# Performance work log

Measured on AMD Instinct MI355X. Metric: run time of the kernel, lower is better.

## Reference

```python
import jax, jax.numpy as jnp
import numpy as np

B, S = 2, 2048
D, H, L = 768, 12, 2
DH = D // H
WIN = 128            # one-sided sliding window
C = WIN              # query chunk size
NC = S // C
FF = 4 * D
V = 50265
SEP_ID = 2
NSEP = 16
G = NSEP + 1         # CLS + all SEP tokens are global
NCLS = 7
HID = 100
NEG = -1e9
SEP_POS = np.arange(1, NSEP + 1) * 120   # fixed [SEP] layout, same every row


def setup_inputs() -> dict:
    key = jax.random.key(0)
    ks = iter(jax.random.split(key, 32))
    def p(shape, scale=0.02):
        return scale * jax.random.normal(next(ks), shape, jnp.float32)
    input_ids = jax.random.randint(next(ks), (B, S), 10, V)
    input_ids = input_ids.at[:, SEP_POS].set(SEP_ID)
    attention_mask = jnp.ones((B, S), jnp.int32)
    return dict(
        input_ids=input_ids, attention_mask=attention_mask,
        tok_emb=p((V, D)), pos_emb=p((S, D)),
        ln_e_g=jnp.ones((D,)), ln_e_b=jnp.zeros((D,)),
        Wq=p((L, D, D)), bq=jnp.zeros((L, D)),
        Wk=p((L, D, D)), bk=jnp.zeros((L, D)),
        Wv=p((L, D, D)), bv=jnp.zeros((L, D)),
        Wo=p((L, D, D)), bo=jnp.zeros((L, D)),
        ln1_g=jnp.ones((L, D)), ln1_b=jnp.zeros((L, D)),
        W1=p((L, D, FF)), b1=jnp.zeros((L, FF)),
        W2=p((L, FF, D)), b2=jnp.zeros((L, D)),
        ln2_g=jnp.ones((L, D)), ln2_b=jnp.zeros((L, D)),
        Wh=p((2 * D, HID)), bh=jnp.zeros((HID,)),
        Wout=p((HID, NCLS)), bout=jnp.zeros((NCLS,)),
    )


def _ln(x, g, b):
    mu = jnp.mean(x, -1, keepdims=True)
    var = jnp.var(x, -1, keepdims=True)
    return (x - mu) * jax.lax.rsqrt(var + 1e-5) * g + b


def forward(input_ids, attention_mask, tok_emb, pos_emb, ln_e_g, ln_e_b,
            Wq, bq, Wk, bk, Wv, bv, Wo, bo, ln1_g, ln1_b,
            W1, b1, W2, b2, ln2_g, ln2_b, Wh, bh, Wout, bout):
    # global positions: CLS + every [SEP] (same layout in every row)
    sep_pos = jnp.nonzero(input_ids[0] == SEP_ID, size=NSEP)[0]          # [NSEP]
    glob = jnp.concatenate([jnp.zeros((1,), sep_pos.dtype), sep_pos])    # [G]

    amask = attention_mask.astype(jnp.float32)                           # [B,S]
    is_glob = jnp.zeros((S,), bool).at[glob].set(True)

    # banded (sliding-window) gather pattern, padded-coordinate indices
    idx = jnp.arange(NC)[:, None] * C + jnp.arange(3 * C)[None, :]       # [NC,3C]
    pos_k = idx - C                                                      # abs key pos
    pos_q = jnp.arange(NC)[:, None] * C + jnp.arange(C)[None, :]         # [NC,C]
    pos_k_c = jnp.clip(pos_k, 0, S - 1)
    band = jnp.abs(pos_k[:, None, :] - pos_q[:, :, None]) <= WIN         # [NC,C,3C]
    inb = (pos_k >= 0) & (pos_k < S)                                     # [NC,3C]
    # global keys are handled by the dedicated global columns -> drop from band
    band = band & (inb & ~is_glob[pos_k_c])[:, None, :]
    km = amask[:, pos_k_c] * inb                                         # [B,NC,3C]
    valid = band[None] & (km[:, :, None, :] > 0)                         # [B,NC,C,3C]
    gmask = amask[:, glob] > 0                                           # [B,G]

    x = tok_emb[input_ids] + pos_emb[None]                               # [B,S,D]
    x = _ln(x, ln_e_g, ln_e_b)

    for l in range(L):
        q = (x @ Wq[l] + bq[l]).reshape(B, S, H, DH).transpose(0, 2, 1, 3) * (DH ** -0.5)
        k = (x @ Wk[l] + bk[l]).reshape(B, S, H, DH).transpose(0, 2, 1, 3)
        v = (x @ Wv[l] + bv[l]).reshape(B, S, H, DH).transpose(0, 2, 1, 3)
        kp = jnp.pad(k, ((0, 0), (0, 0), (C, C), (0, 0)))
        vp = jnp.pad(v, ((0, 0), (0, 0), (C, C), (0, 0)))
        k3 = kp[:, :, idx]                                               # [B,H,NC,3C,DH]
        v3 = vp[:, :, idx]
        qc = q.reshape(B, H, NC, C, DH)
        s_loc = jnp.einsum('bhncd,bhnkd->bhnck', qc, k3)                 # banded scores
        s_loc = jnp.where(valid[:, None], s_loc, NEG)
        kg, vg = k[:, :, glob], v[:, :, glob]                            # [B,H,G,DH]
        s_g = jnp.einsum('bhncd,bhgd->bhncg', qc, kg)
        s_g = jnp.where(gmask[:, None, None, None, :], s_g, NEG)
        p = jax.nn.softmax(jnp.concatenate([s_loc, s_g], axis=-1), axis=-1)
        out = (jnp.einsum('bhnck,bhnkd->bhncd', p[..., :3 * C], v3)
               + jnp.einsum('bhncg,bhgd->bhncd', p[..., 3 * C:], vg))
        out = out.reshape(B, H, S, DH)
        # global query rows attend to the full sequence
        qg = q[:, :, glob]
        s_full = jnp.einsum('bhgd,bhsd->bhgs', qg, k)
        s_full = jnp.where(amask[:, None, None, :] > 0, s_full, NEG)
        out_g = jnp.einsum('bhgs,bhsd->bhgd', jax.nn.softmax(s_full, -1), v)
        out = out.at[:, :, glob, :].set(out_g)
        a = out.transpose(0, 2, 1, 3).reshape(B, S, D) @ Wo[l] + bo[l]
        x = _ln(x + a, ln1_g[l], ln1_b[l])
        h = jax.nn.gelu(x @ W1[l] + b1[l])
        x = _ln(x + h @ W2[l] + b2[l], ln2_g[l], ln2_b[l])

    # core-sentence embeddings: hstack(CLS, interior SEP embeddings)
    core = sep_pos[1:-1]                                                 # [NSEP-2]
    cls = x[:, 0, :]                                                     # [B,D]
    seps = x[:, core, :]                                                 # [B,NSEP-2,D]
    emb = jnp.concatenate([jnp.broadcast_to(cls[:, None], seps.shape), seps], -1)
    emb = emb.reshape(B * (NSEP - 2), 2 * D)
    return jax.nn.relu(emb @ Wh + bh) @ Wout + bout                      # [28, NCLS]


def reference(input_ids, attention_mask, tok_emb, pos_emb, ln_e_g, ln_e_b,
              Wq, bq, Wk, bk, Wv, bv, Wo, bo, ln1_g, ln1_b,
              W1, b1, W2, b2, ln2_g, ln2_b, Wh, bh, Wout, bout):
    return forward(input_ids, attention_mask, tok_emb, pos_emb, ln_e_g, ln_e_b,
                   Wq, bq, Wk, bk, Wv, bv, Wo, bo, ln1_g, ln1_b,
                   W1, b1, W2, b2, ln2_g, ln2_b, Wh, bh, Wout, bout)
```

## Files before the change

### kernel.cpp

```cpp
#include <hip/hip_runtime.h>
#include <hip/hip_bf16.h>
#include <math.h>

#define Sdim 2048
#define Bdim 2
#define Ddim 768
#define Hdim 12
#define DHdim 64
#define Ldim 2
#define Cdim 128
#define NCdim 16
#define FFdim 3072
#define Gdim 17
#define NSEPd 16
#define HIDd 100
#define NCLSd 7
#define SEPID 2
#define MROWS (Bdim*Sdim)
#define QKVS 2304
#define MNSZ (MROWS*Ddim)

typedef __bf16 bf16_t;
typedef bf16_t bf16x8 __attribute__((ext_vector_type(8)));
typedef float f32x4 __attribute__((ext_vector_type(4)));
typedef ushort ushort8v __attribute__((ext_vector_type(8)));

__device__ __forceinline__ ushort f2bf(float f) {
    union { float f; unsigned u; } a; a.f = f;
    unsigned u = a.u;
    unsigned r = (u + 0x7fffu + ((u >> 16) & 1u)) >> 16;
    return (ushort)r;
}
__device__ __forceinline__ float bf2f(ushort h) {
    union { unsigned u; float f; } a; a.u = ((unsigned)h) << 16;
    return a.f;
}
__device__ __forceinline__ void gload16(const ushort* g, ushort* l) {
    __builtin_amdgcn_global_load_lds(
        (const __attribute__((address_space(1))) void*)g,
        (__attribute__((address_space(3))) void*)l, 16, 0, 0);
}

__global__ __launch_bounds__(1024) void k_findsep(const int* __restrict__ ids,
        int* __restrict__ glob, int* __restrict__ isg,
        const float* __restrict__ bq, const float* __restrict__ bk,
        const float* __restrict__ bv, float* __restrict__ bqkv) {
    __shared__ unsigned long long mw[32];
    __shared__ int pfx[32];
    int t = threadIdx.x;
    int flg[2];
    #pragma unroll
    for (int pass = 0; pass < 2; ++pass) {
        int p = pass * 1024 + t;
        int f = (ids[p] == SEPID);
        flg[pass] = f;
        unsigned long long m = __ballot(f);
        if ((t & 63) == 0) mw[pass * 16 + (t >> 6)] = m;
    }
    __syncthreads();
    if (t == 0) {
        int c = 0;
        #pragma unroll
        for (int i = 0; i < 32; ++i) { pfx[i] = c; c += __popcll(mw[i]); }
        glob[0] = 0;
    }
    __syncthreads();
    #pragma unroll
    for (int pass = 0; pass < 2; ++pass) {
        int p = pass * 1024 + t;
        int w = pass * 16 + (t >> 6);
        int lane = t & 63;
        int rank = pfx[w] + __popcll(mw[w] & ((1ull << lane) - 1ull));
        int ig = 0;
        if (flg[pass] && rank < NSEPd) { glob[rank + 1] = p; ig = 1; }
        if (p == 0) ig = 1;
        isg[p] = ig;
    }
    for (int idx = t; idx < Ldim * QKVS; idx += 1024) {
        int l = idx / QKVS, i = idx % QKVS;
        float v = (i < Ddim) ? bq[l * Ddim + i]
                : (i < 2 * Ddim) ? bk[l * Ddim + i - Ddim]
                : bv[l * Ddim + i - 2 * Ddim];
        bqkv[idx] = v;
    }
}

__global__ __launch_bounds__(256) void k_w2bt_all(
        const float* __restrict__ Wq, const float* __restrict__ Wk,
        const float* __restrict__ Wv, const float* __restrict__ Wo,
        const float* __restrict__ W1, const float* __restrict__ W2,
        ushort* __restrict__ wts) {
    const size_t WSMALL = (size_t)Ddim * Ddim;
    const size_t WBIG   = (size_t)Ddim * FFdim;
    const size_t WL     = 4 * WSMALL + 2 * WBIG;
    int bid = blockIdx.x;
    int l = bid / 1728, r = bid % 1728;
    const float* src; ushort* dst; int K, N, tile;
    ushort* base = wts + (size_t)l * WL;
    if (r < 576) {
        int w = r / 144; tile = r % 144; K = Ddim; N = Ddim;
        src = (w == 0 ? Wq : w == 1 ? Wk : w == 2 ? Wv : Wo) + (size_t)l * WSMALL;
        dst = base + (size_t)w * WSMALL;
    } else if (r < 1152) {
        tile = r - 576; K = Ddim; N = FFdim;
        src = W1 + (size_t)l * WBIG; dst = base + 4 * WSMALL;
    } else {
        tile = r - 1152; K = FFdim; N = Ddim;
        src = W2 + (size_t)l * WBIG; dst = base + 4 * WSMALL + WBIG;
    }
    int ntn = N / 64;
    int bn = (tile % ntn) * 64, bk = (tile / ntn) * 64;

    __shared__ float ts[64][65];
    int t = threadIdx.x;
    int rx = t & 63, ry = t >> 6;
    #pragma unroll
    for (int i = 0; i < 16; ++i) {
        int row = ry * 16 + i;
        ts[row][rx] = src[(size_t)(bk + row) * N + bn + rx];
    }
    __syncthreads();
    int wr = t >> 4;
    int k0 = (t & 15) * 4;
    #pragma unroll
    for (int pass = 0; pass < 4; ++pass) {
        int row = pass * 16 + wr;
        ushort4 val;
        val.x = f2bf(ts[k0 + 0][row]);
        val.y = f2bf(ts[k0 + 1][row]);
        val.z = f2bf(ts[k0 + 2][row]);
        val.w = f2bf(ts[k0 + 3][row]);
        *(ushort4*)(&dst[(size_t)(bn + row) * K + bk + k0]) = val;
    }
}

__global__ __launch_bounds__(64) void k_embed(const int* __restrict__ ids,
        const float* __restrict__ tok, const float* __restrict__ pos,
        const float* __restrict__ g, const float* __restrict__ b,
        float* __restrict__ x, ushort* __restrict__ xb) {
    int row = blockIdx.x;
    int s = row & (Sdim - 1);
    long id = ids[row];
    const float4* te = (const float4*)(tok + id * (long)Ddim);
    const float4* pe = (const float4*)(pos + (long)s * Ddim);
    int t = threadIdx.x;
    float4 v[3];
    float ls = 0.f, lq = 0.f;
    #pragma unroll
    for (int i = 0; i < 3; ++i) {
        float4 a = te[i * 64 + t], p = pe[i * 64 + t];
        v[i].x = a.x + p.x; v[i].y = a.y + p.y; v[i].z = a.z + p.z; v[i].w = a.w + p.w;
        ls += v[i].x + v[i].y + v[i].z + v[i].w;
        lq += v[i].x * v[i].x + v[i].y * v[i].y + v[i].z * v[i].z + v[i].w * v[i].w;
    }
    #pragma unroll
    for (int o = 32; o; o >>= 1) { ls += __shfl_xor(ls, o, 64); lq += __shfl_xor(lq, o, 64); }
    float mu = ls / Ddim;
    float var = lq / Ddim - mu * mu;
    float rs = rsqrtf(var + 1e-5f);
    const float4* g4 = (const float4*)g;
    const float4* b4 = (const float4*)b;
    float4* xr = (float4*)(x + (long)row * Ddim);
    ushort4* xbr = (ushort4*)(xb + (long)row * Ddim);
    #pragma unroll
    for (int i = 0; i < 3; ++i) {
        float4 gg = g4[i * 64 + t], bb = b4[i * 64 + t];
        float4 o;
        o.x = (v[i].x - mu) * rs * gg.x + bb.x;
        o.y = (v[i].y - mu) * rs * gg.y + bb.y;
        o.z = (v[i].z - mu) * rs * gg.z + bb.z;
        o.w = (v[i].w - mu) * rs * gg.w + bb.w;
        xr[i * 64 + t] = o;
        ushort4 ob; ob.x = f2bf(o.x); ob.y = f2bf(o.y); ob.z = f2bf(o.z); ob.w = f2bf(o.w);
        xbr[i * 64 + t] = ob;
    }
}

__global__ __launch_bounds__(64) void k_ln_res(float* __restrict__ x,
        const float* __restrict__ a, const float* __restrict__ g,
        const float* __restrict__ b, ushort* __restrict__ xb) {
    long row = blockIdx.x;
    int t = threadIdx.x;
    const float4* xr = (const float4*)(x + row * Ddim);
    const float4* ar = (const float4*)(a + row * Ddim);
    float4 v[3];
    float ls = 0.f, lq = 0.f;
    #pragma unroll
    for (int i = 0; i < 3; ++i) {
        float4 xa = xr[i * 64 + t], aa = ar[i * 64 + t];
        v[i].x = xa.x + aa.x; v[i].y = xa.y + aa.y; v[i].z = xa.z + aa.z; v[i].w = xa.w + aa.w;
        ls += v[i].x + v[i].y + v[i].z + v[i].w;
        lq += v[i].x * v[i].x + v[i].y * v[i].y + v[i].z * v[i].z + v[i].w * v[i].w;
    }
    #pragma unroll
    for (int o = 32; o; o >>= 1) { ls += __shfl_xor(ls, o, 64); lq += __shfl_xor(lq, o, 64); }
    float mu = ls / Ddim;
    float var = lq / Ddim - mu * mu;
    float rs = rsqrtf(var + 1e-5f);
    const float4* g4 = (const float4*)g;
    const float4* b4 = (const float4*)b;
    float4* xw = (float4*)(x + row * Ddim);
    ushort4* xbr = (ushort4*)(xb + row * Ddim);
    #pragma unroll
    for (int i = 0; i < 3; ++i) {
        float4 gg = g4[i * 64 + t], bb = b4[i * 64 + t];
        float4 o;
        o.x = (v[i].x - mu) * rs * gg.x + bb.x;
        o.y = (v[i].y - mu) * rs * gg.y + bb.y;
        o.z = (v[i].z - mu) * rs * gg.z + bb.z;
        o.w = (v[i].w - mu) * rs * gg.w + bb.w;
        xw[i * 64 + t] = o;
        ushort4 ob; ob.x = f2bf(o.x); ob.y = f2bf(o.y); ob.z = f2bf(o.z); ob.w = f2bf(o.w);
        xbr[i * 64 + t] = ob;
    }
}

__global__ __launch_bounds__(64) void k_ln_res4(float* __restrict__ x,
        const float* __restrict__ pr4, const float* __restrict__ bias,
        const float* __restrict__ g, const float* __restrict__ b,
        ushort* __restrict__ xb) {
    long row = blockIdx.x;
    int t = threadIdx.x;
    const float4* xr = (const float4*)(x + row * Ddim);
    const float4* p0 = (const float4*)(pr4 + row * Ddim);
    const float4* p1 = (const float4*)(pr4 + (size_t)MNSZ + row * Ddim);
    const float4* p2 = (const float4*)(pr4 + 2 * (size_t)MNSZ + row * Ddim);
    const float4* p3 = (const float4*)(pr4 + 3 * (size_t)MNSZ + row * Ddim);
    const float4* bi = (const float4*)bias;
    float4 v[3];
    float ls = 0.f, lq = 0.f;
    #pragma unroll
    for (int i = 0; i < 3; ++i) {
        int ii = i * 64 + t;
        float4 xa = xr[ii], a0 = p0[ii], a1 = p1[ii], a2 = p2[ii], a3 = p3[ii], bb = bi[ii];
        v[i].x = xa.x + ((a0.x + a1.x) + (a2.x + a3.x)) + bb.x;
        v[i].y = xa.y + ((a0.y + a1.y) + (a2.y + a3.y)) + bb.y;
        v[i].z = xa.z + ((a0.z + a1.z) + (a2.z + a3.z)) + bb.z;
        v[i].w = xa.w + ((a0.w + a1.w) + (a2.w + a3.w)) + bb.w;
        ls += v[i].x + v[i].y + v[i].z + v[i].w;
        lq += v[i].x * v[i].x + v[i].y * v[i].y + v[i].z * v[i].z + v[i].w * v[i].w;
    }
    #pragma unroll
    for (int o = 32; o; o >>= 1) { ls += __shfl_xor(ls, o, 64); lq += __shfl_xor(lq, o, 64); }
    float mu = ls / Ddim;
    float var = lq / Ddim - mu * mu;
    float rs = rsqrtf(var + 1e-5f);
    const float4* g4 = (const float4*)g;
    const float4* b4 = (const float4*)b;
    float4* xw = (float4*)(x + row * Ddim);
    ushort4* xbr = (ushort4*)(xb + row * Ddim);
    #pragma unroll
    for (int i = 0; i < 3; ++i) {
        float4 gg = g4[i * 64 + t], bb = b4[i * 64 + t];
        float4 o;
        o.x = (v[i].x - mu) * rs * gg.x + bb.x;
        o.y = (v[i].y - mu) * rs * gg.y + bb.y;
        o.z = (v[i].z - mu) * rs * gg.z + bb.z;
        o.w = (v[i].w - mu) * rs * gg.w + bb.w;
        xw[i * 64 + t] = o;
        ushort4 ob; ob.x = f2bf(o.x); ob.y = f2bf(o.y); ob.z = f2bf(o.z); ob.w = f2bf(o.w);
        xbr[i * 64 + t] = ob;
    }
}

template<int ACT, int OUTBF16>
__global__ __launch_bounds__(256) void k_gemm_bf16(
        const ushort* __restrict__ A, const ushort* __restrict__ Wt,
        const float* __restrict__ bias, void* __restrict__ Cout,
        int M, int N, int K)
{
    __shared__ ushort As[128 * 32];
    __shared__ ushort Bs[128 * 32];
    const int t = threadIdx.x;
    const int nwg = gridDim.x * gridDim.y;
    const int wgid = blockIdx.y * gridDim.x + blockIdx.x;
    const int q8 = nwg >> 3, r8 = nwg & 7;
    const int xcd = wgid & 7, idx = wgid >> 3;
    const int swz = (xcd < r8 ? xcd * (q8 + 1) : r8 * (q8 + 1) + (xcd - r8) * q8) + idx;
    const int bm = (swz / gridDim.x) * 128;
    const int bn = (swz % gridDim.x) * 128;
    const int lane = t & 63;
    const int wv = t >> 6;
    const int wm = (wv >> 1) * 64;
    const int wn = (wv & 1) * 64;

    const int srow = t >> 2;
    const int scol = (t & 3) * 8;
    const ushort* gA0 = A + (size_t)(bm + srow) * K + scol;
    const ushort* gA1 = A + (size_t)(bm + 64 + srow) * K + scol;
    const ushort* gB0 = Wt + (size_t)(bn + srow) * K + scol;
    const ushort* gB1 = Wt + (size_t)(bn + 64 + srow) * K + scol;
    ushort* lA0 = As + t * 8;
    ushort* lA1 = As + 2048 + t * 8;
    ushort* lB0 = Bs + t * 8;
    ushort* lB1 = Bs + 2048 + t * 8;

    f32x4 acc[4][4] = {};

    const int frow = lane & 15;
    const int koff = (lane >> 4) * 8;

    for (int k0 = 0; k0 < K; k0 += 32) {
        gload16(gA0 + k0, lA0);
        gload16(gA1 + k0, lA1);
        gload16(gB0 + k0, lB0);
        gload16(gB1 + k0, lB1);
        __syncthreads();
        bf16x8 af[4], bfv[4];
        #pragma unroll
        for (int mi = 0; mi < 4; ++mi)
            af[mi] = *reinterpret_cast<const bf16x8*>(As + (wm + mi * 16 + frow) * 32 + koff);
        #pragma unroll
        for (int ni = 0; ni < 4; ++ni)
            bfv[ni] = *reinterpret_cast<const bf16x8*>(Bs + (wn + ni * 16 + frow) * 32 + koff);
        #pragma unroll
        for (int mi = 0; mi < 4; ++mi)
            #pragma unroll
            for (int ni = 0; ni < 4; ++ni)
                acc[mi][ni] = __builtin_amdgcn_mfma_f32_16x16x32_bf16(af[mi], bfv[ni], acc[mi][ni], 0, 0, 0);
        __syncthreads();
    }
    const int crow0 = (lane >> 4) * 4;
    const int ccol = lane & 15;
    #pragma unroll
    for (int mi = 0; mi < 4; ++mi) {
        #pragma unroll
        for (int ni = 0; ni < 4; ++ni) {
            int gc = bn + wn + ni * 16 + ccol;
            float bv = bias[gc];
            #pragma unroll
            for (int j = 0; j < 4; ++j) {
                int gr = bm + wm + mi * 16 + crow0 + j;
                float v = acc[mi][ni][j] + bv;
                if (ACT == 1) {
                    float y = 0.7978845608f * (v + 0.044715f * v * v * v);
                    float e = __expf(2.f * y);
                    v = v * (1.f - 1.f / (e + 1.f));
                }
                if (OUTBF16) ((ushort*)Cout)[(size_t)gr * N + gc] = f2bf(v);
                else         ((float*)Cout)[(size_t)gr * N + gc] = v;
            }
        }
    }
}

__global__ __launch_bounds__(256) void k_gemm_splitk(
        const ushort* __restrict__ A, const ushort* __restrict__ Wt,
        float* __restrict__ Cpart, int M, int N, int K, int Kper)
{
    __shared__ ushort As[128 * 32];
    __shared__ ushort Bs[128 * 32];
    const int t = threadIdx.x;
    const int ks = blockIdx.z;
    const int nwg = gridDim.x * gridDim.y;
    const int wgid = blockIdx.y * gridDim.x + blockIdx.x;
    const int q8 = nwg >> 3, r8 = nwg & 7;
    const int xcd = wgid & 7, idx = wgid >> 3;
    const int swz = (xcd < r8 ? xcd * (q8 + 1) : r8 * (q8 + 1) + (xcd - r8) * q8) + idx;
    const int bm = (swz / gridDim.x) * 128;
    const int bn = (swz % gridDim.x) * 128;
    const int lane = t & 63;
    const int wv = t >> 6;
    const int wm = (wv >> 1) * 64;
    const int wn = (wv & 1) * 64;

    const int srow = t >> 2;
    const int scol = (t & 3) * 8;
    const int kbase = ks * Kper;
    const ushort* gA0 = A + (size_t)(bm + srow) * K + kbase + scol;
    const ushort* gA1 = A + (size_t)(bm + 64 + srow) * K + kbase + scol;
    const ushort* gB0 = Wt + (size_t)(bn + srow) * K + kbase + scol;
    const ushort* gB1 = Wt + (size_t)(bn + 64 + srow) * K + kbase + scol;
    ushort* lA0 = As + t * 8;
    ushort* lA1 = As + 2048 + t * 8;
    ushort* lB0 = Bs + t * 8;
    ushort* lB1 = Bs + 2048 + t * 8;

    f32x4 acc[4][4] = {};

    const int frow = lane & 15;
    const int koff = (lane >> 4) * 8;

    for (int k0 = 0; k0 < Kper; k0 += 32) {
        gload16(gA0 + k0, lA0);
        gload16(gA1 + k0, lA1);
        gload16(gB0 + k0, lB0);
        gload16(gB1 + k0, lB1);
        __syncthreads();
        bf16x8 af[4], bfv[4];
        #pragma unroll
        for (int mi = 0; mi < 4; ++mi)
            af[mi] = *reinterpret_cast<const bf16x8*>(As + (wm + mi * 16 + frow) * 32 + koff);
        #pragma unroll
        for (int ni = 0; ni < 4; ++ni)
            bfv[ni] = *reinterpret_cast<const bf16x8*>(Bs + (wn + ni * 16 + frow) * 32 + koff);
        #pragma unroll
        for (int mi = 0; mi < 4; ++mi)
            #pragma unroll
            for (int ni = 0; ni < 4; ++ni)
                acc[mi][ni] = __builtin_amdgcn_mfma_f32_16x16x32_bf16(af[mi], bfv[ni], acc[mi][ni], 0, 0, 0);
        __syncthreads();
    }
    float* outp = Cpart + (size_t)ks * M * N;
    const int crow0 = (lane >> 4) * 4;
    const int ccol = lane & 15;
    #pragma unroll
    for (int mi = 0; mi < 4; ++mi) {
        #pragma unroll
        for (int ni = 0; ni < 4; ++ni) {
            int gc = bn + wn + ni * 16 + ccol;
            #pragma unroll
            for (int j = 0; j < 4; ++j) {
                int gr = bm + wm + mi * 16 + crow0 + j;
                outp[(size_t)gr * N + gc] = acc[mi][ni][j];
            }
        }
    }
}

__global__ __launch_bounds__(256) void k_attn_mfma(
        const ushort* __restrict__ qkv, const int* __restrict__ isg,
        const int* __restrict__ glob, const int* __restrict__ amask,
        ushort* __restrict__ ao)
{
    const int n = blockIdx.x, h = blockIdx.y, b = blockIdx.z;
    const int t = threadIdx.x;
    const int lane = t & 63, wv = t >> 6;
    const int R0 = b * Sdim;
    const int l15 = lane & 15, l4 = lane >> 4;

    __shared__ ushort Kb[64 * 64];
    __shared__ ushort Vt[64 * 72];
    __shared__ ushort Plds[4][32 * 72];
    __shared__ float  maskLDS[448];

    for (int i = t; i < 448; i += 256) {
        int ok;
        if (i < 384) {
            int pos = n * Cdim + i - Cdim;
            ok = (pos >= 0 && pos < Sdim);
            if (ok) ok = (amask[b * Sdim + pos] != 0) && (isg[pos] == 0);
        } else {
            int g = i - 384;
            int gp = (g < Gdim) ? glob[g] : 0;
            ok = (g < Gdim) && (amask[b * Sdim + gp] != 0);
        }
        maskLDS[i] = ok ? 0.f : -1e9f;
    }

    bf16x8 qf[2][2];
    #pragma unroll
    for (int qi = 0; qi < 2; ++qi)
        #pragma unroll
        for (int kh = 0; kh < 2; ++kh)
            qf[qi][kh] = *reinterpret_cast<const bf16x8*>(
                qkv + (size_t)(R0 + n * Cdim + wv * 32 + qi * 16 + l15) * QKVS
                    + h * DHdim + kh * 32 + l4 * 8);

    f32x4 accO[2][4] = {};
    float mrow[2][4], lrow[2][4];
    #pragma unroll
    for (int qi = 0; qi < 2; ++qi)
        #pragma unroll
        for (int j = 0; j < 4; ++j) { mrow[qi][j] = -1e30f; lrow[qi][j] = 0.f; }

    const int jj = t >> 3;
    const int c16 = t & 7;

    auto ldone = [&](int j, ushort8v& kr, ushort8v& vr) {
        int pos = 0; bool ok;
        if (j < 384) { pos = n * Cdim + j - Cdim; ok = (pos >= 0 && pos < Sdim); }
        else { int g = j - 384; ok = (g < Gdim); if (ok) pos = glob[g]; }
        ushort8v z = {};
        if (ok) {
            const ushort* kp = qkv + (size_t)(R0 + pos) * QKVS + Ddim + h * DHdim + c16 * 8;
            kr = *reinterpret_cast<const ushort8v*>(kp);
            vr = *reinterpret_cast<const ushort8v*>(kp + Ddim);
        } else { kr = z; vr = z; }
    };

    ushort8v kr0, kr1, vr0, vr1, nk0 = {}, nk1 = {}, nv0 = {}, nv1 = {};
    ldone(jj, kr0, vr0);
    ldone(jj + 32, kr1, vr1);

    for (int kt = 0; kt < 7; ++kt) {
        __syncthreads();
        *reinterpret_cast<ushort8v*>(&Kb[jj * 64 + ((c16 ^ (jj & 7)) * 8)]) = kr0;
        *reinterpret_cast<ushort8v*>(&Kb[(jj + 32) * 64 + ((c16 ^ (jj & 7)) * 8)]) = kr1;
        #pragma unroll
        for (int e = 0; e < 8; ++e) {
            Vt[(c16 * 8 + e) * 72 + jj] = vr0[e];
            Vt[(c16 * 8 + e) * 72 + 32 + jj] = vr1[e];
        }
        if (kt < 6) {
            int base_j = (kt + 1) * 64 + jj;
            ldone(base_j, nk0, nv0);
            ldone(base_j + 32, nk1, nv1);
        }
        __syncthreads();

        bool active = (kt == 6) || ((kt * 64 + 63 >= wv * 32) && (kt * 64 <= wv * 32 + 287));
        if (active) {
            bf16x8 kf[4][2];
            #pragma unroll
            for (int kj = 0; kj < 4; ++kj) {
                int key = kj * 16 + l15;
                #pragma unroll
                for (int kh = 0; kh < 2; ++kh) {
                    int cc = (kh * 4 + l4) ^ (key & 7);
                    kf[kj][kh] = *reinterpret_cast<const bf16x8*>(&Kb[key * 64 + cc * 8]);
                }
            }
            float ma[4];
            #pragma unroll
            for (int kj = 0; kj < 4; ++kj) ma[kj] = maskLDS[kt * 64 + kj * 16 + l15];

            #pragma unroll
            for (int qi = 0; qi < 2; ++qi) {
                f32x4 s[4] = {};
                #pragma unroll
                for (int kj = 0; kj < 4; ++kj)
                    #pragma unroll
                    for (int kh = 0; kh < 2; ++kh)
                        s[kj] = __builtin_amdgcn_mfma_f32_16x16x32_bf16(qf[qi][kh], kf[kj][kh], s[kj], 0, 0, 0);

                float sf[4][4];
                #pragma unroll
                for (int kj = 0; kj < 4; ++kj) {
                    int key = kt * 64 + kj * 16 + l15;
                    #pragma unroll
                    for (int j = 0; j < 4; ++j) {
                        int cq = wv * 32 + qi * 16 + l4 * 4 + j;
                        float sv = s[kj][j] * 0.125f + ma[kj];
                        bool band = (key >= 384) || ((unsigned)(key - cq) <= 256u);
                        sf[kj][j] = band ? sv : sv - 1e9f;
                    }
                }
                float mnew[4], corr[4];
                #pragma unroll
                for (int j = 0; j < 4; ++j) {
                    float v = fmaxf(fmaxf(sf[0][j], sf[1][j]), fmaxf(sf[2][j], sf[3][j]));
                    v = fmaxf(v, __shfl_xor(v, 1, 64));
                    v = fmaxf(v, __shfl_xor(v, 2, 64));
                    v = fmaxf(v, __shfl_xor(v, 4, 64));
                    v = fmaxf(v, __shfl_xor(v, 8, 64));
                    mnew[j] = fmaxf(mrow[qi][j], v);
                    corr[j] = __expf(mrow[qi][j] - mnew[j]);
                    mrow[qi][j] = mnew[j];
                }
                float ps[4][4];
                #pragma unroll
                for (int kj = 0; kj < 4; ++kj)
                    #pragma unroll
                    for (int j = 0; j < 4; ++j)
                        ps[kj][j] = __expf(sf[kj][j] - mnew[j]);
                #pragma unroll
                for (int j = 0; j < 4; ++j) {
                    float r = (ps[0][j] + ps[1][j]) + (ps[2][j] + ps[3][j]);
                    r += __shfl_xor(r, 1, 64);
                    r += __shfl_xor(r, 2, 64);
                    r += __shfl_xor(r, 4, 64);
                    r += __shfl_xor(r, 8, 64);
                    lrow[qi][j] = lrow[qi][j] * corr[j] + r;
                }
                bool need = (corr[0] < 1.f) || (corr[1] < 1.f) || (corr[2] < 1.f) || (corr[3] < 1.f);
                if (__any((int)need)) {
                    #pragma unroll
                    for (int dt = 0; dt < 4; ++dt)
                        #pragma unroll
                        for (int j = 0; j < 4; ++j)
                            accO[qi][dt][j] *= corr[j];
                }
                #pragma unroll
                for (int kj = 0; kj < 4; ++kj)
                    #pragma unroll
                    for (int j = 0; j < 4; ++j)
                        Plds[wv][(qi * 16 + l4 * 4 + j) * 72 + kj * 16 + l15] = f2bf(ps[kj][j]);
            }
            #pragma unroll
            for (int qi = 0; qi < 2; ++qi) {
                #pragma unroll
                for (int ks = 0; ks < 2; ++ks) {
                    bf16x8 af = *reinterpret_cast<const bf16x8*>(
                        &Plds[wv][(qi * 16 + l15) * 72 + ks * 32 + l4 * 8]);
                    #pragma unroll
                    for (int dt = 0; dt < 4; ++dt) {
                        bf16x8 vf = *reinterpret_cast<const bf16x8*>(
                            &Vt[(dt * 16 + l15) * 72 + ks * 32 + l4 * 8]);
                        accO[qi][dt] = __builtin_amdgcn_mfma_f32_16x16x32_bf16(af, vf, accO[qi][dt], 0, 0, 0);
                    }
                }
            }
        }
        kr0 = nk0; kr1 = nk1; vr0 = nv0; vr1 = nv1;
    }

    #pragma unroll
    for (int qi = 0; qi < 2; ++qi) {
        float inv[4];
        #pragma unroll
        for (int j = 0; j < 4; ++j) inv[j] = 1.f / lrow[qi][j];
        #pragma unroll
        for (int dt = 0; dt < 4; ++dt) {
            #pragma unroll
            for (int j = 0; j < 4; ++j) {
                int crow = n * Cdim + wv * 32 + qi * 16 + l4 * 4 + j;
                ao[(size_t)(R0 + crow) * Ddim + h * DHdim + dt * 16 + l15] =
                    f2bf(accO[qi][dt][j] * inv[j]);
            }
        }
    }
}

__global__ __launch_bounds__(256) void k_attn_glob(const ushort* __restrict__ qkv,
        const int* __restrict__ glob, const int* __restrict__ amask,
        ushort* __restrict__ ao) {
    int g = blockIdx.x, h = blockIdx.y, b = blockIdx.z;
    __shared__ float sc[Sdim];
    __shared__ float qs[DHdim];
    __shared__ float redm[4], reds[4];
    __shared__ float part[32][DHdim];
    int t = threadIdx.x;
    int qr = glob[g];
    const int R0 = b * Sdim;
    if (t < DHdim)
        qs[t] = bf2f(qkv[(size_t)(R0 + qr) * QKVS + h * DHdim + t]) * 0.125f;
    __syncthreads();
    float lm = -1e30f;
    for (int s0 = t; s0 < Sdim; s0 += 256) {
        const ushort8v* kr = (const ushort8v*)(qkv + (size_t)(R0 + s0) * QKVS + Ddim + h * DHdim);
        float s = 0.f;
        #pragma unroll
        for (int cc = 0; cc < 8; ++cc) {
            ushort8v kv = kr[cc];
            #pragma unroll
            for (int e = 0; e < 8; ++e) s += qs[cc * 8 + e] * bf2f(kv[e]);
        }
        if (amask[b * Sdim + s0] == 0) s = -1e30f;
        sc[s0] = s;
        lm = fmaxf(lm, s);
    }
    #pragma unroll
    for (int o = 32; o; o >>= 1) lm = fmaxf(lm, __shfl_xor(lm, o, 64));
    if ((t & 63) == 0) redm[t >> 6] = lm;
    __syncthreads();
    float mx = fmaxf(fmaxf(redm[0], redm[1]), fmaxf(redm[2], redm[3]));
    float lsum = 0.f;
    for (int s0 = t; s0 < Sdim; s0 += 256) {
        float p = __expf(sc[s0] - mx);
        sc[s0] = p; lsum += p;
    }
    #pragma unroll
    for (int o = 32; o; o >>= 1) lsum += __shfl_xor(lsum, o, 64);
    if ((t & 63) == 0) reds[t >> 6] = lsum;
    __syncthreads();
    float l = reds[0] + reds[1] + reds[2] + reds[3];
    int chunk = t >> 3, dg = t & 7;
    float a[8] = {};
    for (int r = chunk * 64; r < chunk * 64 + 64; ++r) {
        float p = sc[r];
        ushort8v vv = *(const ushort8v*)(qkv + (size_t)(R0 + r) * QKVS + 2 * Ddim + h * DHdim + dg * 8);
        #pragma unroll
        for (int e = 0; e < 8; ++e) a[e] += p * bf2f(vv[e]);
    }
    #pragma unroll
    for (int e = 0; e < 8; ++e) part[chunk][dg * 8 + e] = a[e];
    __syncthreads();
    if (t < DHdim) {
        float o = 0.f;
        #pragma unroll
        for (int c = 0; c < 32; ++c) o += part[c][t];
        ao[(size_t)(R0 + qr) * Ddim + h * DHdim + t] = f2bf(o / l);
    }
}

__global__ __launch_bounds__(256) void k_head(const float* __restrict__ x,
        const int* __restrict__ glob, const float* __restrict__ Wh,
        const float* __restrict__ bh, const float* __restrict__ Wout,
        const float* __restrict__ bout, float* __restrict__ out) {
    int i = blockIdx.x;
    int b = i / 14, j = i % 14;
    __shared__ float emb[2 * Ddim];
    __shared__ float hp[2][128];
    __shared__ float hid[HIDd];
    int t = threadIdx.x;
    int p = glob[j + 2];
    for (int d = t; d < Ddim; d += 256) {
        emb[d] = x[(long)b * Sdim * Ddim + d];
        emb[Ddim + d] = x[((long)b * Sdim + p) * Ddim + d];
    }
    __syncthreads();
    int nn = t & 127, half = t >> 7;
    float s = 0.f;
    if (nn < HIDd) {
        int k0 = half * Ddim;
        for (int k1 = 0; k1 < Ddim; ++k1) s += emb[k0 + k1] * Wh[(k0 + k1) * HIDd + nn];
    }
    hp[half][nn] = s;
    __syncthreads();
    if (t < HIDd) hid[t] = fmaxf(hp[0][t] + hp[1][t] + bh[t], 0.f);
    __syncthreads();
    if (t < NCLSd) {
        float s2 = bout[t];
        for (int o = 0; o < HIDd; ++o) s2 += hid[o] * Wout[o * NCLSd + t];
        out[i * NCLSd + t] = s2;
    }
}

extern "C" void kernel_launch(void* const* d_in, const int* in_sizes, int n_in,
                              void* d_out, int out_size, void* d_ws, size_t ws_size,
                              hipStream_t stream) {
    const int*   ids   = (const int*)d_in[0];
    const int*   am    = (const int*)d_in[1];
    const float* tok   = (const float*)d_in[2];
    const float* pos   = (const float*)d_in[3];
    const float* lneg  = (const float*)d_in[4];
    const float* lneb  = (const float*)d_in[5];
    const float* Wq    = (const float*)d_in[6];
    const float* bq    = (const float*)d_in[7];
    const float* Wk    = (const float*)d_in[8];
    const float* bk    = (const float*)d_in[9];
    const float* Wv    = (const float*)d_in[10];
    const float* bv    = (const float*)d_in[11];
    const float* Wo    = (const float*)d_in[12];
    const float* bo    = (const float*)d_in[13];
    const float* ln1g  = (const float*)d_in[14];
    const float* ln1b  = (const float*)d_in[15];
    const float* W1    = (const float*)d_in[16];
    const float* b1    = (const float*)d_in[17];
    const float* W2    = (const float*)d_in[18];
    const float* b2    = (const float*)d_in[19];
    const float* ln2g  = (const float*)d_in[20];
    const float* ln2b  = (const float*)d_in[21];
    const float* Wh    = (const float*)d_in[22];
    const float* bh    = (const float*)d_in[23];
    const float* Wout  = (const float*)d_in[24];
    const float* bout  = (const float*)d_in[25];
    float* out = (float*)d_out;

    char* ws = (char*)d_ws;
    const size_t SZ = (size_t)MROWS * Ddim * sizeof(float);
    const size_t HB = SZ / 2;
    size_t off = 0;
    float*  x    = (float*)(ws + off);  off += SZ;
    float*  pr4  = (float*)(ws + off);  off += 4 * SZ;
    ushort* xb   = (ushort*)(ws + off); off += HB;
    ushort* qkvB = (ushort*)(ws + off); off += (size_t)MROWS * QKVS * 2;
    ushort* aoB  = (ushort*)(ws + off); off += HB;
    ushort* hh   = (ushort*)(ws + off); off += (size_t)MROWS * FFdim * 2;
    const size_t WSMALL = (size_t)Ddim * Ddim;
    const size_t WBIG   = (size_t)Ddim * FFdim;
    const size_t WL     = 4 * WSMALL + 2 * WBIG;
    ushort* wts = (ushort*)(ws + off); off += WL * Ldim * 2;
    float* bqkv = (float*)(ws + off);  off += Ldim * QKVS * sizeof(float);
    int* glob = (int*)(ws + off); off += 256;
    int* isg  = (int*)(ws + off);

    k_findsep<<<1, 1024, 0, stream>>>(ids, glob, isg, bq, bk, bv, bqkv);
    k_w2bt_all<<<3456, 256, 0, stream>>>(Wq, Wk, Wv, Wo, W1, W2, wts);
    k_embed<<<MROWS, 64, 0, stream>>>(ids, tok, pos, lneg, lneb, x, xb);

    dim3 g768(Ddim / 128, MROWS / 128);
    dim3 gQKV(QKVS / 128, MROWS / 128);
    dim3 gFF(FFdim / 128, MROWS / 128);
    dim3 gW2(Ddim / 128, MROWS / 128, 4);
    dim3 gloc(NCdim, Hdim, Bdim);
    dim3 gglb(Gdim, Hdim, Bdim);

    for (int l = 0; l < Ldim; ++l) {
        ushort* base = wts + l * WL;
        ushort* Wqkvt = base;
        ushort* Wot = base + 3 * WSMALL;
        ushort* W1t = base + 4 * WSMALL;
        ushort* W2t = base + 4 * WSMALL + WBIG;
        k_gemm_bf16<0,1><<<gQKV, 256, 0, stream>>>(xb, Wqkvt, bqkv + l * QKVS, qkvB, MROWS, QKVS, Ddim);
        k_attn_mfma<<<gloc, 256, 0, stream>>>(qkvB, isg, glob, am, aoB);
        k_attn_glob<<<gglb, 256, 0, stream>>>(qkvB, glob, am, aoB);
        k_gemm_bf16<0,0><<<g768, 256, 0, stream>>>(aoB, Wot, bo + l * Ddim, pr4, MROWS, Ddim, Ddim);
        k_ln_res<<<MROWS, 64, 0, stream>>>(x, pr4, ln1g + l * Ddim, ln1b + l * Ddim, xb);
        k_gemm_bf16<1,1><<<gFF, 256, 0, stream>>>(xb, W1t, b1 + l * FFdim, hh, MROWS, FFdim, Ddim);
        k_gemm_splitk<<<gW2, 256, 0, stream>>>(hh, W2t, pr4, MROWS, Ddim, FFdim, FFdim / 4);
        k_ln_res4<<<MROWS, 64, 0, stream>>>(x, pr4, b2 + l * Ddim, ln2g + l * Ddim, ln2b + l * Ddim, xb);
    }
    k_head<<<Bdim * (NSEPd - 2), 256, 0, stream>>>(x, glob, Wh, bh, Wout, bout, out);
}
```

Measured before the change: 486.0 us.

## Double-buffer GEMM LDS staging and split-K the attention output projection

Both GEMM kernels now use two LDS buffers per operand. The next K-slice is loaded while MFMAs run on the current one, and each iteration needs one barrier instead of two. The Wo projection now uses the 4-way split-K kernel, with bias and residual folded into the 4-partial layernorm kernel, so more workgroups run on the small 768-wide GEMM. The cost is twice the LDS per workgroup, which may reduce occupancy, plus extra partial-sum traffic for the Wo output.

```diff
diff --git a/kernel.cpp b/kernel.cpp
--- a/kernel.cpp
+++ b/kernel.cpp
@@ -176,45 +176,6 @@
     }
 }
 
-__global__ __launch_bounds__(64) void k_ln_res(float* __restrict__ x,
-        const float* __restrict__ a, const float* __restrict__ g,
-        const float* __restrict__ b, ushort* __restrict__ xb) {
-    long row = blockIdx.x;
-    int t = threadIdx.x;
-    const float4* xr = (const float4*)(x + row * Ddim);
-    const float4* ar = (const float4*)(a + row * Ddim);
-    float4 v[3];
-    float ls = 0.f, lq = 0.f;
-    #pragma unroll
-    for (int i = 0; i < 3; ++i) {
-        float4 xa = xr[i * 64 + t], aa = ar[i * 64 + t];
-        v[i].x = xa.x + aa.x; v[i].y = xa.y + aa.y; v[i].z = xa.z + aa.z; v[i].w = xa.w + aa.w;
-        ls += v[i].x + v[i].y + v[i].z + v[i].w;
-        lq += v[i].x * v[i].x + v[i].y * v[i].y + v[i].z * v[i].z + v[i].w * v[i].w;
-    }
-    #pragma unroll
-    for (int o = 32; o; o >>= 1) { ls += __shfl_xor(ls, o, 64); lq += __shfl_xor(lq, o, 64); }
-    float mu = ls / Ddim;
-    float var = lq / Ddim - mu * mu;
-    float rs = rsqrtf(var + 1e-5f);
-    const float4* g4 = (const float4*)g;
-    const float4* b4 = (const float4*)b;
-    float4* xw = (float4*)(x + row * Ddim);
-    ushort4* xbr = (ushort4*)(xb + row * Ddim);
-    #pragma unroll
-    for (int i = 0; i < 3; ++i) {
-        float4 gg = g4[i * 64 + t], bb = b4[i * 64 + t];
-        float4 o;
-        o.x = (v[i].x - mu) * rs * gg.x + bb.x;
-        o.y = (v[i].y - mu) * rs * gg.y + bb.y;
-        o.z = (v[i].z - mu) * rs * gg.z + bb.z;
-        o.w = (v[i].w - mu) * rs * gg.w + bb.w;
-        xw[i * 64 + t] = o;
-        ushort4 ob; ob.x = f2bf(o.x); ob.y = f2bf(o.y); ob.z = f2bf(o.z); ob.w = f2bf(o.w);
-        xbr[i * 64 + t] = ob;
-    }
-}
-
 __global__ __launch_bounds__(64) void k_ln_res4(float* __restrict__ x,
         const float* __restrict__ pr4, const float* __restrict__ bias,
         const float* __restrict__ g, const float* __restrict__ b,
@@ -269,8 +230,8 @@
         const float* __restrict__ bias, void* __restrict__ Cout,
         int M, int N, int K)
 {
-    __shared__ ushort As[128 * 32];
-    __shared__ ushort Bs[128 * 32];
+    __shared__ ushort As[2][128 * 32];
+    __shared__ ushort Bs[2][128 * 32];
     const int t = threadIdx.x;
     const int nwg = gridDim.x * gridDim.y;
     const int wgid = blockIdx.y * gridDim.x + blockIdx.x;
@@ -290,35 +251,38 @@
     const ushort* gA1 = A + (size_t)(bm + 64 + srow) * K + scol;
     const ushort* gB0 = Wt + (size_t)(bn + srow) * K + scol;
     const ushort* gB1 = Wt + (size_t)(bn + 64 + srow) * K + scol;
-    ushort* lA0 = As + t * 8;
-    ushort* lA1 = As + 2048 + t * 8;
-    ushort* lB0 = Bs + t * 8;
-    ushort* lB1 = Bs + 2048 + t * 8;
 
     f32x4 acc[4][4] = {};
-
     const int frow = lane & 15;
     const int koff = (lane >> 4) * 8;
 
-    for (int k0 = 0; k0 < K; k0 += 32) {
-        gload16(gA0 + k0, lA0);
-        gload16(gA1 + k0, lA1);
-        gload16(gB0 + k0, lB0);
-        gload16(gB1 + k0, lB1);
-        __syncthreads();
+    auto stage = [&](int d, int k0) {
+        gload16(gA0 + k0, &As[d][t * 8]);
+        gload16(gA1 + k0, &As[d][2048 + t * 8]);
+        gload16(gB0 + k0, &Bs[d][t * 8]);
+        gload16(gB1 + k0, &Bs[d][2048 + t * 8]);
+    };
+
+    stage(0, 0);
+    __syncthreads();
+    const int niter = K / 32;
+    int cur = 0;
+    for (int it = 0; it < niter; ++it) {
+        if (it + 1 < niter) stage(cur ^ 1, (it + 1) * 32);
         bf16x8 af[4], bfv[4];
         #pragma unroll
         for (int mi = 0; mi < 4; ++mi)
-            af[mi] = *reinterpret_cast<const bf16x8*>(As + (wm + mi * 16 + frow) * 32 + koff);
+            af[mi] = *reinterpret_cast<const bf16x8*>(&As[cur][(wm + mi * 16 + frow) * 32 + koff]);
         #pragma unroll
         for (int ni = 0; ni < 4; ++ni)
-            bfv[ni] = *reinterpret_cast<const bf16x8*>(Bs + (wn + ni * 16 + frow) * 32 + koff);
+            bfv[ni] = *reinterpret_cast<const bf16x8*>(&Bs[cur][(wn + ni * 16 + frow) * 32 + koff]);
         #pragma unroll
         for (int mi = 0; mi < 4; ++mi)
             #pragma unroll
             for (int ni = 0; ni < 4; ++ni)
                 acc[mi][ni] = __builtin_amdgcn_mfma_f32_16x16x32_bf16(af[mi], bfv[ni], acc[mi][ni], 0, 0, 0);
         __syncthreads();
+        cur ^= 1;
     }
     const int crow0 = (lane >> 4) * 4;
     const int ccol = lane & 15;
@@ -348,8 +312,8 @@
         const ushort* __restrict__ A, const ushort* __restrict__ Wt,
         float* __restrict__ Cpart, int M, int N, int K, int Kper)
 {
-    __shared__ ushort As[128 * 32];
-    __shared__ ushort Bs[128 * 32];
+    __shared__ ushort As[2][128 * 32];
+    __shared__ ushort Bs[2][128 * 32];
     const int t = threadIdx.x;
     const int ks = blockIdx.z;
     const int nwg = gridDim.x * gridDim.y;
@@ -371,35 +335,38 @@
     const ushort* gA1 = A + (size_t)(bm + 64 + srow) * K + kbase + scol;
     const ushort* gB0 = Wt + (size_t)(bn + srow) * K + kbase + scol;
     const ushort* gB1 = Wt + (size_t)(bn + 64 + srow) * K + kbase + scol;
-    ushort* lA0 = As + t * 8;
-    ushort* lA1 = As + 2048 + t * 8;
-    ushort* lB0 = Bs + t * 8;
-    ushort* lB1 = Bs + 2048 + t * 8;
 
     f32x4 acc[4][4] = {};
-
     const int frow = lane & 15;
     const int koff = (lane >> 4) * 8;
 
-    for (int k0 = 0; k0 < Kper; k0 += 32) {
-        gload16(gA0 + k0, lA0);
-        gload16(gA1 + k0, lA1);
-        gload16(gB0 + k0, lB0);
-        gload16(gB1 + k0, lB1);
-        __syncthreads();
+    auto stage = [&](int d, int k0) {
+        gload16(gA0 + k0, &As[d][t * 8]);
+        gload16(gA1 + k0, &As[d][2048 + t * 8]);
+        gload16(gB0 + k0, &Bs[d][t * 8]);
+        gload16(gB1 + k0, &Bs[d][2048 + t * 8]);
+    };
+
+    stage(0, 0);
+    __syncthreads();
+    const int niter = Kper / 32;
+    int cur = 0;
+    for (int it = 0; it < niter; ++it) {
+        if (it + 1 < niter) stage(cur ^ 1, (it + 1) * 32);
         bf16x8 af[4], bfv[4];
         #pragma unroll
         for (int mi = 0; mi < 4; ++mi)
-            af[mi] = *reinterpret_cast<const bf16x8*>(As + (wm + mi * 16 + frow) * 32 + koff);
+            af[mi] = *reinterpret_cast<const bf16x8*>(&As[cur][(wm + mi * 16 + frow) * 32 + koff]);
         #pragma unroll
         for (int ni = 0; ni < 4; ++ni)
-            bfv[ni] = *reinterpret_cast<const bf16x8*>(Bs + (wn + ni * 16 + frow) * 32 + koff);
+            bfv[ni] = *reinterpret_cast<const bf16x8*>(&Bs[cur][(wn + ni * 16 + frow) * 32 + koff]);
         #pragma unroll
         for (int mi = 0; mi < 4; ++mi)
             #pragma unroll
             for (int ni = 0; ni < 4; ++ni)
                 acc[mi][ni] = __builtin_amdgcn_mfma_f32_16x16x32_bf16(af[mi], bfv[ni], acc[mi][ni], 0, 0, 0);
         __syncthreads();
+        cur ^= 1;
     }
     float* outp = Cpart + (size_t)ks * M * N;
     const int crow0 = (lane >> 4) * 4;
@@ -760,10 +727,9 @@
     k_w2bt_all<<<3456, 256, 0, stream>>>(Wq, Wk, Wv, Wo, W1, W2, wts);
     k_embed<<<MROWS, 64, 0, stream>>>(ids, tok, pos, lneg, lneb, x, xb);
 
-    dim3 g768(Ddim / 128, MROWS / 128);
     dim3 gQKV(QKVS / 128, MROWS / 128);
     dim3 gFF(FFdim / 128, MROWS / 128);
-    dim3 gW2(Ddim / 128, MROWS / 128, 4);
+    dim3 gSK(Ddim / 128, MROWS / 128, 4);
     dim3 gloc(NCdim, Hdim, Bdim);
     dim3 gglb(Gdim, Hdim, Bdim);
 
@@ -776,10 +742,10 @@
         k_gemm_bf16<0,1><<<gQKV, 256, 0, stream>>>(xb, Wqkvt, bqkv + l * QKVS, qkvB, MROWS, QKVS, Ddim);
         k_attn_mfma<<<gloc, 256, 0, stream>>>(qkvB, isg, glob, am, aoB);
         k_attn_glob<<<gglb, 256, 0, stream>>>(qkvB, glob, am, aoB);
-        k_gemm_bf16<0,0><<<g768, 256, 0, stream>>>(aoB, Wot, bo + l * Ddim, pr4, MROWS, Ddim, Ddim);
-        k_ln_res<<<MROWS, 64, 0, stream>>>(x, pr4, ln1g + l * Ddim, ln1b + l * Ddim, xb);
+        k_gemm_splitk<<<gSK, 256, 0, stream>>>(aoB, Wot, pr4, MROWS, Ddim, Ddim, Ddim / 4);
+        k_ln_res4<<<MROWS, 64, 0, stream>>>(x, pr4, bo + l * Ddim, ln1g + l * Ddim, ln1b + l * Ddim, xb);
         k_gemm_bf16<1,1><<<gFF, 256, 0, stream>>>(xb, W1t, b1 + l * FFdim, hh, MROWS, FFdim, Ddim);
-        k_gemm_splitk<<<gW2, 256, 0, stream>>>(hh, W2t, pr4, MROWS, Ddim, FFdim, FFdim / 4);
+        k_gemm_splitk<<<gSK, 256, 0, stream>>>(hh, W2t, pr4, MROWS, Ddim, FFdim, FFdim / 4);
         k_ln_res4<<<MROWS, 64, 0, stream>>>(x, pr4, b2 + l * Ddim, ln2g + l * Ddim, ln2b + l * Ddim, xb);
     }
     k_head<<<Bdim * (NSEPd - 2), 256, 0, stream>>>(x, glob, Wh, bh, Wout, bout, out);
```

Result: faster. 473.5 us (median of 2 runs) (-2.6%).
